# Performance work log

Measured on AMD Instinct MI355X. Metric: run time of the kernel, lower is better.

Reference implementation:

```python
import jax, jax.numpy as jnp
import numpy as np

N, E, D, H, C, L, G, LATENT = 50000, 800000, 128, 8, 16, 3, 100, 64
NEG_SLOPE = 0.2
BN_EPS = 1e-5


def gat_layer(x, src, dst, W, a_src, a_dst, b):
    # x: [N, D] -> h: [N, H, C]
    h = (x @ W).reshape(N, H, C)
    # per-node attention logits, gathered per edge
    alpha_src = jnp.einsum('nhc,hc->nh', h, a_src)  # [N, H]
    alpha_dst = jnp.einsum('nhc,hc->nh', h, a_dst)  # [N, H]
    e = jax.nn.leaky_relu(alpha_src[src] + alpha_dst[dst], NEG_SLOPE)  # [E', H]
    # segment softmax over destination node (self-loops guarantee non-empty segments)
    m = jax.ops.segment_max(e, dst, num_segments=N)          # [N, H]
    ex = jnp.exp(e - m[dst])
    denom = jax.ops.segment_sum(ex, dst, num_segments=N)     # [N, H]
    alpha = ex / (denom[dst] + 1e-16)                        # [E', H]
    msg = h[src] * alpha[:, :, None]                         # [E', H, C]
    out = jax.ops.segment_sum(msg, dst, num_segments=N)      # [N, H, C]
    return out.reshape(N, H * C) + b


def setup_inputs() -> dict:
    key = jax.random.key(0)
    ks = jax.random.split(key, 12)
    x = jax.random.normal(ks[0], (N, D), dtype=jnp.float32)
    edge_index = jax.random.randint(ks[1], (2, E), 0, N, dtype=jnp.int32)
    batch = jnp.sort(jax.random.randint(ks[2], (N,), 0, G, dtype=jnp.int32))
    s = 1.0 / np.sqrt(D)
    W = jax.random.uniform(ks[3], (L, D, H * C), jnp.float32, -s, s)
    att_src = jax.random.uniform(ks[4], (L, H, C), jnp.float32, -s, s)
    att_dst = jax.random.uniform(ks[5], (L, H, C), jnp.float32, -s, s)
    bias = jnp.zeros((L, H * C), jnp.float32)
    bn_gamma = jnp.ones((H * C,), jnp.float32)
    bn_beta = jnp.zeros((H * C,), jnp.float32)
    sf = 1.0 / np.sqrt(H * C)
    fc_w = jax.random.uniform(ks[6], (LATENT, H * C), jnp.float32, -sf, sf)
    fc_b = jax.random.uniform(ks[7], (LATENT,), jnp.float32, -sf, sf)
    return dict(x=x, edge_index=edge_index, batch=batch, W=W, att_src=att_src,
                att_dst=att_dst, bias=bias, bn_gamma=bn_gamma, bn_beta=bn_beta,
                fc_w=fc_w, fc_b=fc_b)


def reference(x, edge_index, batch, W, att_src, att_dst, bias, bn_gamma, bn_beta, fc_w, fc_b):
    # add self-loops (PyG GATConv default add_self_loops=True)
    loops = jnp.arange(N, dtype=edge_index.dtype)
    src = jnp.concatenate([edge_index[0], loops])
    dst = jnp.concatenate([edge_index[1], loops])
    h = x
    for l in range(L):
        h = gat_layer(h, src, dst, W[l], att_src[l], att_dst[l], bias[l])
        h = jax.nn.elu(h)  # dropout is identity in eval mode
    # global add pool over graphs
    pooled = jax.ops.segment_sum(h, batch, num_segments=G)  # [G, H*C]
    # BatchNorm1d with batch statistics (training-mode math)
    mu = pooled.mean(axis=0)
    var = pooled.var(axis=0)
    normed = (pooled - mu) * jax.lax.rsqrt(var + BN_EPS) * bn_gamma + bn_beta
    return normed @ fc_w.T + fc_b
```

## Files before the change

kernel.cpp:

```cpp
#include <hip/hip_runtime.h>
#include <cstdint>
#include <cstddef>

#define N_NODES 50000
#define N_EDGES 800000
#define N_ETOT  850000
#define DIM     128
#define NHEAD   8
#define NGRAPH  100
#define NLAT    64
#define NEG_SLOPE 0.2f
#define BN_EPS  1e-5f

#define NBUCKET 196
#define CAP     5120
#define EPB     4096
#define POOL_CHUNK 50

typedef unsigned int   u32;
typedef unsigned short u16;

__device__ __forceinline__ float b2f(u16 u){
    union { u32 i; float f; } v; v.i = ((u32)u) << 16; return v.f;
}
__device__ __forceinline__ u16 f2b(float f){
    union { float f; u32 i; } v; v.f = f;
    u32 u = v.i;
    u32 r = (u + 0x7fffu + ((u >> 16) & 1u)) >> 16;
    return (u16)r;
}


__launch_bounds__(256)
__global__ void k_bin(const int* __restrict__ ei, int* __restrict__ bucket_cur,
                      u32* __restrict__ binned){
    __shared__ u32 stage[EPB];
    __shared__ int hist[256], scanb[256], curb[256], gbase[256];
    const int tid = threadIdx.x;
    const int e0  = blockIdx.x * EPB;

    hist[tid] = 0;
    __syncthreads();

    #pragma unroll
    for (int j = 0; j < EPB / 256; j++) {
        int e = e0 + j * 256 + tid;
        if (e < N_ETOT) {
            int d = (e < N_EDGES) ? ei[N_EDGES + e] : (e - N_EDGES);
            atomicAdd(&hist[d >> 8], 1);
        }
    }
    __syncthreads();

    __shared__ int s[256];
    s[tid] = hist[tid];
    __syncthreads();
    for (int o = 1; o < 256; o <<= 1) {
        int t = (tid >= o) ? s[tid - o] : 0;
        __syncthreads();
        s[tid] += t;
        __syncthreads();
    }
    scanb[tid] = s[tid] - hist[tid];
    curb[tid]  = 0;
    __syncthreads();

    #pragma unroll
    for (int j = 0; j < EPB / 256; j++) {
        int e = e0 + j * 256 + tid;
        if (e < N_ETOT) {
            int src, d;
            if (e < N_EDGES) { src = ei[e]; d = ei[N_EDGES + e]; }
            else             { src = e - N_EDGES; d = src; }
            int b = d >> 8;
            int r = atomicAdd(&curb[b], 1);
            stage[scanb[b] + r] = (u32)src | ((u32)(d & 255) << 16) | ((u32)b << 24);
        }
    }
    __syncthreads();

    if (tid < NBUCKET && hist[tid] > 0)
        gbase[tid] = atomicAdd(&bucket_cur[tid], hist[tid]);
    __syncthreads();

    int nvalid = min(EPB, N_ETOT - e0);
    for (int i = tid; i < nvalid; i += 256) {
        u32 rec = stage[i];
        int b = rec >> 24;
        int pos = gbase[b] + (i - scanb[b]);
        if (pos < CAP) binned[(size_t)b * CAP + pos] = rec;
    }
}

__launch_bounds__(256)
__global__ void k_bucket(const int* __restrict__ bucket_cur, const u32* __restrict__ binned,
                         int* __restrict__ rowbeg, int* __restrict__ rowend,
                         int* __restrict__ csr){
    __shared__ int deg[256], off[256], cur[256], s[256];
    const int tid = threadIdx.x;
    const int b   = blockIdx.x;
    const int cnt = min(bucket_cur[b], CAP);
    const int base = b * CAP;

    deg[tid] = 0;
    __syncthreads();
    for (int i = tid; i < cnt; i += 256)
        atomicAdd(&deg[(binned[base + i] >> 16) & 255], 1);
    __syncthreads();

    s[tid] = deg[tid];
    __syncthreads();
    for (int o = 1; o < 256; o <<= 1) {
        int t = (tid >= o) ? s[tid - o] : 0;
        __syncthreads();
        s[tid] += t;
        __syncthreads();
    }
    off[tid] = s[tid] - deg[tid];
    cur[tid] = s[tid] - deg[tid];
    __syncthreads();

    int node = b * 256 + tid;
    if (node < N_NODES) {
        rowbeg[node] = base + off[tid];
        rowend[node] = base + off[tid] + deg[tid];
    }

    for (int i = tid; i < cnt; i += 256) {
        u32 rec = binned[base + i];
        int l = (rec >> 16) & 255;
        int p = atomicAdd(&cur[l], 1);
        csr[base + p] = (int)(rec & 0xffffu);
    }
}


__device__ __forceinline__ void gemm_body(const float* __restrict__ W,
                                          const float* __restrict__ asrc,
                                          const float* __restrict__ adst,
                                          u16* __restrict__ hp,
                                          float* __restrict__ as_, float* __restrict__ ad_,
                                          float* xs, int r0, int tid){
    const int cq = tid & 31;
    const int rg = tid >> 5;
    float acc[8][4];
    #pragma unroll
    for (int r = 0; r < 8; r++)
        #pragma unroll
        for (int c = 0; c < 4; c++) acc[r][c] = 0.f;

    for (int k = 0; k < 128; k += 4) {
        float4 w0 = *(const float4*)(W + (k + 0) * 128 + 4 * cq);
        float4 w1 = *(const float4*)(W + (k + 1) * 128 + 4 * cq);
        float4 w2 = *(const float4*)(W + (k + 2) * 128 + 4 * cq);
        float4 w3 = *(const float4*)(W + (k + 3) * 128 + 4 * cq);
        #pragma unroll
        for (int rr = 0; rr < 8; rr++) {
            float4 xv = *(const float4*)(xs + (rg * 8 + rr) * 128 + k);
            acc[rr][0] = fmaf(xv.x, w0.x, acc[rr][0]);
            acc[rr][1] = fmaf(xv.x, w0.y, acc[rr][1]);
            acc[rr][2] = fmaf(xv.x, w0.z, acc[rr][2]);
            acc[rr][3] = fmaf(xv.x, w0.w, acc[rr][3]);
            acc[rr][0] = fmaf(xv.y, w1.x, acc[rr][0]);
            acc[rr][1] = fmaf(xv.y, w1.y, acc[rr][1]);
            acc[rr][2] = fmaf(xv.y, w1.z, acc[rr][2]);
            acc[rr][3] = fmaf(xv.y, w1.w, acc[rr][3]);
            acc[rr][0] = fmaf(xv.z, w2.x, acc[rr][0]);
            acc[rr][1] = fmaf(xv.z, w2.y, acc[rr][1]);
            acc[rr][2] = fmaf(xv.z, w2.z, acc[rr][2]);
            acc[rr][3] = fmaf(xv.z, w2.w, acc[rr][3]);
            acc[rr][0] = fmaf(xv.w, w3.x, acc[rr][0]);
            acc[rr][1] = fmaf(xv.w, w3.y, acc[rr][1]);
            acc[rr][2] = fmaf(xv.w, w3.z, acc[rr][2]);
            acc[rr][3] = fmaf(xv.w, w3.w, acc[rr][3]);
        }
    }

    const int h  = cq >> 2;
    const int c0 = (cq & 3) * 4;
    const float4 av = *(const float4*)(asrc + h * 16 + c0);
    const float4 bv = *(const float4*)(adst + h * 16 + c0);

    #pragma unroll
    for (int rr = 0; rr < 8; rr++) {
        int row = r0 + rg * 8 + rr;
        if (row < N_NODES) {
            uint2 p;
            p.x = (u32)f2b(acc[rr][0]) | ((u32)f2b(acc[rr][1]) << 16);
            p.y = (u32)f2b(acc[rr][2]) | ((u32)f2b(acc[rr][3]) << 16);
            *(uint2*)(hp + (size_t)row * 128 + 4 * cq) = p;
        }
        float s0 = acc[rr][0] * av.x + acc[rr][1] * av.y + acc[rr][2] * av.z + acc[rr][3] * av.w;
        float s1 = acc[rr][0] * bv.x + acc[rr][1] * bv.y + acc[rr][2] * bv.z + acc[rr][3] * bv.w;
        s0 += __shfl_xor(s0, 1); s0 += __shfl_xor(s0, 2);
        s1 += __shfl_xor(s1, 1); s1 += __shfl_xor(s1, 2);
        if ((cq & 3) == 0 && row < N_NODES) {
            as_[(size_t)row * 8 + h] = s0;
            ad_[(size_t)row * 8 + h] = s1;
        }
    }
}

__launch_bounds__(256)
__global__ void k_gemm_f32(const float* __restrict__ x, const float* __restrict__ W,
                           const float* __restrict__ asrc, const float* __restrict__ adst,
                           u16* __restrict__ hp,
                           float* __restrict__ as_, float* __restrict__ ad_){
    __shared__ float xs[64 * 128];
    const int tid = threadIdx.x;
    const int r0  = blockIdx.x * 64;
    for (int c = tid; c < 2048; c += 256) {
        int row = r0 + (c >> 5);
        float4 v = make_float4(0.f, 0.f, 0.f, 0.f);
        if (row < N_NODES) v = *(const float4*)(x + (size_t)row * 128 + (c & 31) * 4);
        *(float4*)(xs + c * 4) = v;
    }
    __syncthreads();
    gemm_body(W, asrc, adst, hp, as_, ad_, xs, r0, tid);
}

__launch_bounds__(256)
__global__ void k_gemm_bf16(const u16* __restrict__ x, const float* __restrict__ W,
                            const float* __restrict__ asrc, const float* __restrict__ adst,
                            u16* __restrict__ hp,
                            float* __restrict__ as_, float* __restrict__ ad_){
    __shared__ float xs[64 * 128];
    const int tid = threadIdx.x;
    const int r0  = blockIdx.x * 64;
    for (int c = tid; c < 1024; c += 256) {
        int row = r0 + (c >> 4);
        uint4 v = make_uint4(0, 0, 0, 0);
        if (row < N_NODES) v = *(const uint4*)(x + (size_t)row * 128 + (c & 15) * 8);
        float* d = xs + (c >> 4) * 128 + (c & 15) * 8;
        d[0] = b2f((u16)(v.x & 0xffff)); d[1] = b2f((u16)(v.x >> 16));
        d[2] = b2f((u16)(v.y & 0xffff)); d[3] = b2f((u16)(v.y >> 16));
        d[4] = b2f((u16)(v.z & 0xffff)); d[5] = b2f((u16)(v.z >> 16));
        d[6] = b2f((u16)(v.w & 0xffff)); d[7] = b2f((u16)(v.w >> 16));
    }
    __syncthreads();
    gemm_body(W, asrc, adst, hp, as_, ad_, xs, r0, tid);
}


__launch_bounds__(256)
__global__ void k_agg(const int* __restrict__ rowbeg, const int* __restrict__ rowend,
                      const int* __restrict__ csr,
                      const float* __restrict__ as_, const float* __restrict__ ad_,
                      const uint4* __restrict__ hp4, const float* __restrict__ bias,
                      u16* __restrict__ xout){
    const int lane = threadIdx.x & 63;
    const int wid  = threadIdx.x >> 6;
    const int n    = blockIdx.x * 4 + wid;
    if (n >= N_NODES) return;
    const int beg = rowbeg[n], end = rowend[n];

    const int q  = lane >> 4;
    const int li = lane & 15;
    const int h  = li >> 1;
    const float adn = ad_[(size_t)n * 8 + h];

    float acc[8];
    #pragma unroll
    for (int j = 0; j < 8; j++) acc[j] = 0.f;
    float den = 0.f;

    for (int e0 = beg; e0 < end; e0 += 8) {
        int eA = e0 + q, eB = e0 + 4 + q;
        int sA = csr[min(eA, end - 1)];
        int sB = csr[min(eB, end - 1)];
        float vA = as_[(size_t)sA * 8 + h] + adn;
        float vB = as_[(size_t)sB * 8 + h] + adn;
        uint4 pA = hp4[(size_t)sA * 16 + li];
        uint4 pB = hp4[(size_t)sB * 16 + li];
        vA = vA > 0.f ? vA : NEG_SLOPE * vA;
        vB = vB > 0.f ? vB : NEG_SLOPE * vB;
        float wA = (eA < end) ? __expf(vA) : 0.f;
        float wB = (eB < end) ? __expf(vB) : 0.f;
        den += wA + wB;
        acc[0] = fmaf(wA, b2f((u16)(pA.x & 0xffff)), acc[0]);
        acc[1] = fmaf(wA, b2f((u16)(pA.x >> 16)),    acc[1]);
        acc[2] = fmaf(wA, b2f((u16)(pA.y & 0xffff)), acc[2]);
        acc[3] = fmaf(wA, b2f((u16)(pA.y >> 16)),    acc[3]);
        acc[4] = fmaf(wA, b2f((u16)(pA.z & 0xffff)), acc[4]);
        acc[5] = fmaf(wA, b2f((u16)(pA.z >> 16)),    acc[5]);
        acc[6] = fmaf(wA, b2f((u16)(pA.w & 0xffff)), acc[6]);
        acc[7] = fmaf(wA, b2f((u16)(pA.w >> 16)),    acc[7]);
        acc[0] = fmaf(wB, b2f((u16)(pB.x & 0xffff)), acc[0]);
        acc[1] = fmaf(wB, b2f((u16)(pB.x >> 16)),    acc[1]);
        acc[2] = fmaf(wB, b2f((u16)(pB.y & 0xffff)), acc[2]);
        acc[3] = fmaf(wB, b2f((u16)(pB.y >> 16)),    acc[3]);
        acc[4] = fmaf(wB, b2f((u16)(pB.z & 0xffff)), acc[4]);
        acc[5] = fmaf(wB, b2f((u16)(pB.z >> 16)),    acc[5]);
        acc[6] = fmaf(wB, b2f((u16)(pB.w & 0xffff)), acc[6]);
        acc[7] = fmaf(wB, b2f((u16)(pB.w >> 16)),    acc[7]);
    }

    #pragma unroll
    for (int j = 0; j < 8; j++) {
        acc[j] += __shfl_xor(acc[j], 16);
        acc[j] += __shfl_xor(acc[j], 32);
    }
    den += __shfl_xor(den, 16);
    den += __shfl_xor(den, 32);

    if (q == 0) {
        const float inv = 1.f / (den + 1e-16f);
        const float4 b0 = *(const float4*)(bias + 8 * li);
        const float4 b1 = *(const float4*)(bias + 8 * li + 4);
        float o[8];
        o[0] = acc[0] * inv + b0.x; o[1] = acc[1] * inv + b0.y;
        o[2] = acc[2] * inv + b0.z; o[3] = acc[3] * inv + b0.w;
        o[4] = acc[4] * inv + b1.x; o[5] = acc[5] * inv + b1.y;
        o[6] = acc[6] * inv + b1.z; o[7] = acc[7] * inv + b1.w;
        #pragma unroll
        for (int j = 0; j < 8; j++)
            o[j] = o[j] > 0.f ? o[j] : (__expf(o[j]) - 1.f);
        uint4 p;
        p.x = (u32)f2b(o[0]) | ((u32)f2b(o[1]) << 16);
        p.y = (u32)f2b(o[2]) | ((u32)f2b(o[3]) << 16);
        p.z = (u32)f2b(o[4]) | ((u32)f2b(o[5]) << 16);
        p.w = (u32)f2b(o[6]) | ((u32)f2b(o[7]) << 16);
        *(uint4*)(xout + (size_t)n * 128 + 8 * li) = p;
    }
}


__global__ void k_pool(const u16* __restrict__ x, const int* __restrict__ batch,
                       float* __restrict__ pooled){
    int tid = threadIdx.x;
    int n0 = blockIdx.x * POOL_CHUNK;
    int nend = min(n0 + POOL_CHUNK, N_NODES);
    float acc = 0.f;
    int cur = batch[n0];
    for (int n = n0; n < nend; n++) {
        int g = batch[n];
        if (g != cur) {
            atomicAdd(&pooled[cur * 128 + tid], acc);
            acc = 0.f; cur = g;
        }
        acc += b2f(x[(size_t)n * 128 + tid]);
    }
    atomicAdd(&pooled[cur * 128 + tid], acc);
}

__launch_bounds__(256)
__global__ void k_bn(const float* __restrict__ pooled, const float* __restrict__ gamma,
                     const float* __restrict__ beta, float* __restrict__ normed){
    const int lane = threadIdx.x & 63;
    const int f    = blockIdx.x * 4 + (threadIdx.x >> 6);
    const int g1 = lane, g2 = lane + 64;
    float v1 = (g1 < NGRAPH) ? pooled[g1 * 128 + f] : 0.f;
    float v2 = (g2 < NGRAPH) ? pooled[g2 * 128 + f] : 0.f;

    float s = v1 + v2;
    #pragma unroll
    for (int o = 1; o < 64; o <<= 1) s += __shfl_xor(s, o);
    const float mu = s * (1.f / NGRAPH);

    float d1 = (g1 < NGRAPH) ? (v1 - mu) : 0.f;
    float d2 = (g2 < NGRAPH) ? (v2 - mu) : 0.f;
    float q = d1 * d1 + d2 * d2;
    #pragma unroll
    for (int o = 1; o < 64; o <<= 1) q += __shfl_xor(q, o);
    const float rs = rsqrtf(q * (1.f / NGRAPH) + BN_EPS);

    const float ga = gamma[f], be = beta[f];
    if (g1 < NGRAPH) normed[g1 * 128 + f] = d1 * rs * ga + be;
    if (g2 < NGRAPH) normed[g2 * 128 + f] = d2 * rs * ga + be;
}

__launch_bounds__(64)
__global__ void k_fc(const float* __restrict__ normed, const float* __restrict__ fw,
                     const float* __restrict__ fb, float* __restrict__ out){
    const int g = blockIdx.x, j = threadIdx.x;
    float acc = fb[j];
    const float4* wr = (const float4*)(fw + j * 128);
    const float4* nr = (const float4*)(normed + g * 128);
    #pragma unroll
    for (int k = 0; k < 32; k++) {
        float4 w = wr[k], n4 = nr[k];
        acc = fmaf(n4.x, w.x, acc);
        acc = fmaf(n4.y, w.y, acc);
        acc = fmaf(n4.z, w.z, acc);
        acc = fmaf(n4.w, w.w, acc);
    }
    out[g * 64 + j] = acc;
}


extern "C" void kernel_launch(void* const* d_in, const int* in_sizes, int n_in,
                              void* d_out, int out_size, void* d_ws, size_t ws_size,
                              hipStream_t stream) {
    const float* x0    = (const float*)d_in[0];
    const int*   ei    = (const int*)d_in[1];
    const int*   batch = (const int*)d_in[2];
    const float* Wp    = (const float*)d_in[3];
    const float* asrc  = (const float*)d_in[4];
    const float* adst  = (const float*)d_in[5];
    const float* bias  = (const float*)d_in[6];
    const float* gamma = (const float*)d_in[7];
    const float* beta  = (const float*)d_in[8];
    const float* fw    = (const float*)d_in[9];
    const float* fb    = (const float*)d_in[10];
    float* out = (float*)d_out;

    char* w = (char*)d_ws;
    size_t off = 0;
    auto take = [&](size_t bytes) -> char* {
        char* p = w + off;
        off += (bytes + 255) & ~(size_t)255;
        return p;
    };
    int*   rowbeg  = (int*)take((size_t)N_NODES * 4);
    int*   rowend  = (int*)take((size_t)N_NODES * 4);
    int*   bucket_cur = (int*)take(NBUCKET * 4);
    u32*   binned  = (u32*)take((size_t)NBUCKET * CAP * 4);
    int*   csr     = (int*)take((size_t)NBUCKET * CAP * 4);
    u16*   hp      = (u16*)take((size_t)N_NODES * 128 * 2);
    float* as_     = (float*)take((size_t)N_NODES * 8 * 4);
    float* ad_     = (float*)take((size_t)N_NODES * 8 * 4);
    u16*   xb1     = (u16*)take((size_t)N_NODES * 128 * 2);
    u16*   xb2     = (u16*)take((size_t)N_NODES * 128 * 2);
    float* pooled  = (float*)take((size_t)NGRAPH * 128 * 4);
    float* normed  = (float*)take((size_t)NGRAPH * 128 * 4);

    hipMemsetAsync(bucket_cur, 0, NBUCKET * 4, stream);
    hipMemsetAsync(pooled, 0, (size_t)NGRAPH * 128 * 4, stream);

    k_bin   <<<(N_ETOT + EPB - 1) / EPB, 256, 0, stream>>>(ei, bucket_cur, binned);
    k_bucket<<<NBUCKET, 256, 0, stream>>>(bucket_cur, binned, rowbeg, rowend, csr);

    const int gblk = (N_NODES + 63) / 64;
    const int ablk = (N_NODES + 3) / 4;

    k_gemm_f32<<<gblk, 256, 0, stream>>>(x0, Wp, asrc, adst, hp, as_, ad_);
    k_agg<<<ablk, 256, 0, stream>>>(rowbeg, rowend, csr, as_, ad_,
                                    (const uint4*)hp, bias, xb1);
    k_gemm_bf16<<<gblk, 256, 0, stream>>>(xb1, Wp + (size_t)1 * 128 * 128,
                                          asrc + 128, adst + 128, hp, as_, ad_);
    k_agg<<<ablk, 256, 0, stream>>>(rowbeg, rowend, csr, as_, ad_,
                                    (const uint4*)hp, bias + 128, xb2);
    k_gemm_bf16<<<gblk, 256, 0, stream>>>(xb2, Wp + (size_t)2 * 128 * 128,
                                          asrc + 256, adst + 256, hp, as_, ad_);
    k_agg<<<ablk, 256, 0, stream>>>(rowbeg, rowend, csr, as_, ad_,
                                    (const uint4*)hp, bias + 256, xb1);

    k_pool<<<(N_NODES + POOL_CHUNK - 1) / POOL_CHUNK, 128, 0, stream>>>(xb1, batch, pooled);
    k_bn<<<32, 256, 0, stream>>>(pooled, gamma, beta, normed);
    k_fc<<<NGRAPH, NLAT, 0, stream>>>(normed, fw, fb, out);
}
```

Before: 358.5 us.

## Replace scalar FP32 GEMM with bf16 MFMA GEMM using pretransposed bf16 weights

Adds a small kernel that converts and transposes each layer's weight matrix to bf16 once. The per-layer projection GEMM is rewritten to stage bf16 inputs and weights in padded LDS and run 16x16x32 bf16 MFMA instructions instead of scalar FMAs. The attention logits are then computed from the bf16-rounded outputs staged in LDS. This targets the FP32 ALU cost of the projection at the price of bf16 rounding of the first-layer input and weights, and a larger LDS footprint per block.

Result: faster. 312.4 us (-12.9%).

```diff
diff --git a/kernel.cpp b/kernel.cpp
--- a/kernel.cpp
+++ b/kernel.cpp
@@ -17,8 +17,12 @@
 #define EPB     4096
 #define POOL_CHUNK 50
 
+#define XSTR 136
+
 typedef unsigned int   u32;
 typedef unsigned short u16;
+typedef short  bf16x8 __attribute__((ext_vector_type(8)));
+typedef float  f32x4  __attribute__((ext_vector_type(4)));
 
 __device__ __forceinline__ float b2f(u16 u){
     union { u32 i; float f; } v; v.i = ((u32)u) << 16; return v.f;
@@ -135,110 +139,112 @@
 }
 
 
-__device__ __forceinline__ void gemm_body(const float* __restrict__ W,
-                                          const float* __restrict__ asrc,
-                                          const float* __restrict__ adst,
-                                          u16* __restrict__ hp,
-                                          float* __restrict__ as_, float* __restrict__ ad_,
-                                          float* xs, int r0, int tid){
-    const int cq = tid & 31;
-    const int rg = tid >> 5;
-    float acc[8][4];
-    #pragma unroll
-    for (int r = 0; r < 8; r++)
-        #pragma unroll
-        for (int c = 0; c < 4; c++) acc[r][c] = 0.f;
-
-    for (int k = 0; k < 128; k += 4) {
-        float4 w0 = *(const float4*)(W + (k + 0) * 128 + 4 * cq);
-        float4 w1 = *(const float4*)(W + (k + 1) * 128 + 4 * cq);
-        float4 w2 = *(const float4*)(W + (k + 2) * 128 + 4 * cq);
-        float4 w3 = *(const float4*)(W + (k + 3) * 128 + 4 * cq);
-        #pragma unroll
-        for (int rr = 0; rr < 8; rr++) {
-            float4 xv = *(const float4*)(xs + (rg * 8 + rr) * 128 + k);
-            acc[rr][0] = fmaf(xv.x, w0.x, acc[rr][0]);
-            acc[rr][1] = fmaf(xv.x, w0.y, acc[rr][1]);
-            acc[rr][2] = fmaf(xv.x, w0.z, acc[rr][2]);
-            acc[rr][3] = fmaf(xv.x, w0.w, acc[rr][3]);
-            acc[rr][0] = fmaf(xv.y, w1.x, acc[rr][0]);
-            acc[rr][1] = fmaf(xv.y, w1.y, acc[rr][1]);
-            acc[rr][2] = fmaf(xv.y, w1.z, acc[rr][2]);
-            acc[rr][3] = fmaf(xv.y, w1.w, acc[rr][3]);
-            acc[rr][0] = fmaf(xv.z, w2.x, acc[rr][0]);
-            acc[rr][1] = fmaf(xv.z, w2.y, acc[rr][1]);
-            acc[rr][2] = fmaf(xv.z, w2.z, acc[rr][2]);
-            acc[rr][3] = fmaf(xv.z, w2.w, acc[rr][3]);
-            acc[rr][0] = fmaf(xv.w, w3.x, acc[rr][0]);
-            acc[rr][1] = fmaf(xv.w, w3.y, acc[rr][1]);
-            acc[rr][2] = fmaf(xv.w, w3.z, acc[rr][2]);
-            acc[rr][3] = fmaf(xv.w, w3.w, acc[rr][3]);
-        }
-    }
-
-    const int h  = cq >> 2;
-    const int c0 = (cq & 3) * 4;
-    const float4 av = *(const float4*)(asrc + h * 16 + c0);
-    const float4 bv = *(const float4*)(adst + h * 16 + c0);
-
-    #pragma unroll
-    for (int rr = 0; rr < 8; rr++) {
-        int row = r0 + rg * 8 + rr;
-        if (row < N_NODES) {
-            uint2 p;
-            p.x = (u32)f2b(acc[rr][0]) | ((u32)f2b(acc[rr][1]) << 16);
-            p.y = (u32)f2b(acc[rr][2]) | ((u32)f2b(acc[rr][3]) << 16);
-            *(uint2*)(hp + (size_t)row * 128 + 4 * cq) = p;
-        }
-        float s0 = acc[rr][0] * av.x + acc[rr][1] * av.y + acc[rr][2] * av.z + acc[rr][3] * av.w;
-        float s1 = acc[rr][0] * bv.x + acc[rr][1] * bv.y + acc[rr][2] * bv.z + acc[rr][3] * bv.w;
-        s0 += __shfl_xor(s0, 1); s0 += __shfl_xor(s0, 2);
-        s1 += __shfl_xor(s1, 1); s1 += __shfl_xor(s1, 2);
-        if ((cq & 3) == 0 && row < N_NODES) {
-            as_[(size_t)row * 8 + h] = s0;
-            ad_[(size_t)row * 8 + h] = s1;
-        }
-    }
-}
-
-__launch_bounds__(256)
-__global__ void k_gemm_f32(const float* __restrict__ x, const float* __restrict__ W,
-                           const float* __restrict__ asrc, const float* __restrict__ adst,
-                           u16* __restrict__ hp,
-                           float* __restrict__ as_, float* __restrict__ ad_){
-    __shared__ float xs[64 * 128];
+__launch_bounds__(256)
+__global__ void k_wt(const float* __restrict__ Wp, u16* __restrict__ wt_g){
+    int task = blockIdx.x * 256 + threadIdx.x;
+    if (task >= 3 * 128 * 16) return;
+    int layer = task >> 11;
+    int rem   = task & 2047;
+    int n  = rem >> 4;
+    int kc = rem & 15;
+    const float* src = Wp + layer * 16384;
+    u16 tmp[8];
+    #pragma unroll
+    for (int j = 0; j < 8; j++)
+        tmp[j] = f2b(src[(kc * 8 + j) * 128 + n]);
+    *(uint4*)(wt_g + (size_t)layer * 16384 + n * 128 + kc * 8) = *(uint4*)tmp;
+}
+
+
+template<bool BF16IN>
+__launch_bounds__(256)
+__global__ void k_gemm(const void* __restrict__ xin, const u16* __restrict__ wt_g,
+                       const float* __restrict__ asrc, const float* __restrict__ adst,
+                       u16* __restrict__ hp,
+                       float* __restrict__ as_, float* __restrict__ ad_){
+    __shared__ u16 xs[64 * XSTR];
+    __shared__ u16 wt[128 * XSTR];
     const int tid = threadIdx.x;
     const int r0  = blockIdx.x * 64;
-    for (int c = tid; c < 2048; c += 256) {
-        int row = r0 + (c >> 5);
-        float4 v = make_float4(0.f, 0.f, 0.f, 0.f);
-        if (row < N_NODES) v = *(const float4*)(x + (size_t)row * 128 + (c & 31) * 4);
-        *(float4*)(xs + c * 4) = v;
-    }
-    __syncthreads();
-    gemm_body(W, asrc, adst, hp, as_, ad_, xs, r0, tid);
-}
-
-__launch_bounds__(256)
-__global__ void k_gemm_bf16(const u16* __restrict__ x, const float* __restrict__ W,
-                            const float* __restrict__ asrc, const float* __restrict__ adst,
-                            u16* __restrict__ hp,
-                            float* __restrict__ as_, float* __restrict__ ad_){
-    __shared__ float xs[64 * 128];
-    const int tid = threadIdx.x;
-    const int r0  = blockIdx.x * 64;
-    for (int c = tid; c < 1024; c += 256) {
-        int row = r0 + (c >> 4);
-        uint4 v = make_uint4(0, 0, 0, 0);
-        if (row < N_NODES) v = *(const uint4*)(x + (size_t)row * 128 + (c & 15) * 8);
-        float* d = xs + (c >> 4) * 128 + (c & 15) * 8;
-        d[0] = b2f((u16)(v.x & 0xffff)); d[1] = b2f((u16)(v.x >> 16));
-        d[2] = b2f((u16)(v.y & 0xffff)); d[3] = b2f((u16)(v.y >> 16));
-        d[4] = b2f((u16)(v.z & 0xffff)); d[5] = b2f((u16)(v.z >> 16));
-        d[6] = b2f((u16)(v.w & 0xffff)); d[7] = b2f((u16)(v.w >> 16));
-    }
-    __syncthreads();
-    gemm_body(W, asrc, adst, hp, as_, ad_, xs, r0, tid);
+
+    for (int c = tid; c < 128 * 16; c += 256) {
+        int n = c >> 4, ch = c & 15;
+        *(uint4*)(wt + n * XSTR + ch * 8) = *(const uint4*)(wt_g + n * 128 + ch * 8);
+    }
+    if (BF16IN) {
+        const u16* x = (const u16*)xin;
+        for (int c = tid; c < 64 * 16; c += 256) {
+            int row = r0 + (c >> 4);
+            uint4 v = make_uint4(0, 0, 0, 0);
+            if (row < N_NODES) v = *(const uint4*)(x + (size_t)row * 128 + (c & 15) * 8);
+            *(uint4*)(xs + (c >> 4) * XSTR + (c & 15) * 8) = v;
+        }
+    } else {
+        const float* x = (const float*)xin;
+        for (int c = tid; c < 64 * 16; c += 256) {
+            int row = r0 + (c >> 4);
+            u16 t[8] = {0,0,0,0,0,0,0,0};
+            if (row < N_NODES) {
+                const float* p = x + (size_t)row * 128 + (c & 15) * 8;
+                #pragma unroll
+                for (int j = 0; j < 8; j++) t[j] = f2b(p[j]);
+            }
+            *(uint4*)(xs + (c >> 4) * XSTR + (c & 15) * 8) = *(uint4*)t;
+        }
+    }
+    __syncthreads();
+
+    const int lane = tid & 63;
+    const int wv   = tid >> 6;
+    const int m    = lane & 15;
+    const int quad = lane >> 4;
+
+    const u16* arow = xs + (16 * wv + m) * XSTR + quad * 8;
+    bf16x8 a0 = *(const bf16x8*)(arow);
+    bf16x8 a1 = *(const bf16x8*)(arow + 32);
+    bf16x8 a2 = *(const bf16x8*)(arow + 64);
+    bf16x8 a3 = *(const bf16x8*)(arow + 96);
+
+    #pragma unroll
+    for (int c = 0; c < 8; c++) {
+        const u16* brow = wt + (16 * c + m) * XSTR + quad * 8;
+        f32x4 acc = {0.f, 0.f, 0.f, 0.f};
+        acc = __builtin_amdgcn_mfma_f32_16x16x32_bf16(a0, *(const bf16x8*)(brow),      acc, 0, 0, 0);
+        acc = __builtin_amdgcn_mfma_f32_16x16x32_bf16(a1, *(const bf16x8*)(brow + 32), acc, 0, 0, 0);
+        acc = __builtin_amdgcn_mfma_f32_16x16x32_bf16(a2, *(const bf16x8*)(brow + 64), acc, 0, 0, 0);
+        acc = __builtin_amdgcn_mfma_f32_16x16x32_bf16(a3, *(const bf16x8*)(brow + 96), acc, 0, 0, 0);
+        u16* orow = xs + (16 * wv + quad * 4) * XSTR + 16 * c + m;
+        orow[0]        = f2b(acc[0]);
+        orow[XSTR]     = f2b(acc[1]);
+        orow[2 * XSTR] = f2b(acc[2]);
+        orow[3 * XSTR] = f2b(acc[3]);
+    }
+    __syncthreads();
+
+    for (int t = tid; t < 512; t += 256) {
+        int row = t >> 3, h = t & 7;
+        int gr = r0 + row;
+        if (gr >= N_NODES) continue;
+        const u16* hr = xs + row * XSTR + h * 16;
+        const float* av = asrc + h * 16;
+        const float* bv = adst + h * 16;
+        float s0 = 0.f, s1 = 0.f;
+        #pragma unroll
+        for (int j = 0; j < 16; j++) {
+            float v = b2f(hr[j]);
+            s0 = fmaf(v, av[j], s0);
+            s1 = fmaf(v, bv[j], s1);
+        }
+        as_[(size_t)gr * 8 + h] = s0;
+        ad_[(size_t)gr * 8 + h] = s1;
+    }
+
+    for (int t = tid; t < 1024; t += 256) {
+        int row = t >> 4, ch = t & 15;
+        int gr = r0 + row;
+        if (gr >= N_NODES) continue;
+        *(uint4*)(hp + (size_t)gr * 128 + ch * 8) = *(const uint4*)(xs + row * XSTR + ch * 8);
+    }
 }
 
 
@@ -416,6 +422,7 @@
     int*   bucket_cur = (int*)take(NBUCKET * 4);
     u32*   binned  = (u32*)take((size_t)NBUCKET * CAP * 4);
     int*   csr     = (int*)take((size_t)NBUCKET * CAP * 4);
+    u16*   wt_g    = (u16*)take((size_t)3 * 128 * 128 * 2);
     u16*   hp      = (u16*)take((size_t)N_NODES * 128 * 2);
     float* as_     = (float*)take((size_t)N_NODES * 8 * 4);
     float* ad_     = (float*)take((size_t)N_NODES * 8 * 4);
@@ -428,20 +435,21 @@
     hipMemsetAsync(pooled, 0, (size_t)NGRAPH * 128 * 4, stream);
 
     k_bin   <<<(N_ETOT + EPB - 1) / EPB, 256, 0, stream>>>(ei, bucket_cur, binned);
+    k_wt    <<<24, 256, 0, stream>>>(Wp, wt_g);
     k_bucket<<<NBUCKET, 256, 0, stream>>>(bucket_cur, binned, rowbeg, rowend, csr);
 
     const int gblk = (N_NODES + 63) / 64;
     const int ablk = (N_NODES + 3) / 4;
 
-    k_gemm_f32<<<gblk, 256, 0, stream>>>(x0, Wp, asrc, adst, hp, as_, ad_);
+    k_gemm<false><<<gblk, 256, 0, stream>>>(x0, wt_g, asrc, adst, hp, as_, ad_);
     k_agg<<<ablk, 256, 0, stream>>>(rowbeg, rowend, csr, as_, ad_,
                                     (const uint4*)hp, bias, xb1);
-    k_gemm_bf16<<<gblk, 256, 0, stream>>>(xb1, Wp + (size_t)1 * 128 * 128,
-                                          asrc + 128, adst + 128, hp, as_, ad_);
+    k_gemm<true><<<gblk, 256, 0, stream>>>(xb1, wt_g + 16384, asrc + 128, adst + 128,
+                                           hp, as_, ad_);
     k_agg<<<ablk, 256, 0, stream>>>(rowbeg, rowend, csr, as_, ad_,
                                     (const uint4*)hp, bias + 128, xb2);
-    k_gemm_bf16<<<gblk, 256, 0, stream>>>(xb2, Wp + (size_t)2 * 128 * 128,
-                                          asrc + 256, adst + 256, hp, as_, ad_);
+    k_gemm<true><<<gblk, 256, 0, stream>>>(xb2, wt_g + 32768, asrc + 256, adst + 256,
+                                           hp, as_, ad_);
     k_agg<<<ablk, 256, 0, stream>>>(rowbeg, rowend, csr, as_, ad_,
                                     (const uint4*)hp, bias + 256, xb1);
 
```
